# Kernel tuning notes

Hardware: AMD Instinct MI355X
Metric: run time of the kernel (lower is better)

Reference implementation:

```python
import jax, jax.numpy as jnp
import numpy as np

NUM_EMB = 16384
EMB_DIM = 64
BETA = 0.25  # commitment_cost, legacy=True formulation


def _l2norm(x, axis=-1):
    # matches F.normalize(p=2): x / max(||x||, 1e-12)
    n = jnp.sqrt(jnp.sum(x * x, axis=axis, keepdims=True))
    return x / jnp.maximum(n, 1e-12)


def setup_inputs() -> dict:
    key = jax.random.key(0)
    k_z, k_cb, k_w, k_b = jax.random.split(key, 4)
    z = jax.random.normal(k_z, (16, 1024, EMB_DIM), dtype=jnp.float32)
    # frozen codebook: N(0, d^{-0.5})
    codebook = jax.random.normal(k_cb, (NUM_EMB, EMB_DIM), dtype=jnp.float32) * (EMB_DIM ** -0.5)
    # Linear(d, d) default init: U(-1/sqrt(d), 1/sqrt(d))
    lim = 1.0 / np.sqrt(EMB_DIM)
    proj_w = jax.random.uniform(k_w, (EMB_DIM, EMB_DIM), dtype=jnp.float32, minval=-lim, maxval=lim)
    proj_b = jax.random.uniform(k_b, (EMB_DIM,), dtype=jnp.float32, minval=-lim, maxval=lim)
    scale = jnp.float32(10.0)  # l2_norm_scale
    return {"z": z, "codebook": codebook, "proj_w": proj_w, "proj_b": proj_b, "scale": scale}


def reference(z, codebook, proj_w, proj_b, scale):
    B, T, d = z.shape
    zf = z.reshape(-1, d)                                   # [BT, d]
    quant_codebook = codebook @ proj_w.T + proj_b           # [N, d]
    zn = _l2norm(zf)
    cn = _l2norm(quant_codebook)
    distances = -jnp.einsum('bd,nd->bn', zn, cn) * scale    # [BT, N]
    idx = jnp.argmin(distances, axis=1)                     # [BT]
    quantized = quant_codebook[idx].reshape(z.shape)        # [B, T, d]
    sg = jax.lax.stop_gradient
    commitment_loss = jnp.mean((sg(quantized) - z) ** 2)
    codebook_loss = jnp.mean((quantized - sg(z)) ** 2)
    vq_loss = commitment_loss + BETA * codebook_loss        # legacy=True
    quantized_st = z + sg(quantized - z)                    # straight-through
    return quantized_st, vq_loss, idx.reshape(B, T)
```

## Files before the change

### kernel.cpp

```cpp
#include <hip/hip_runtime.h>
#include <hip/hip_bf16.h>


#define NCODES 16384
#define NTOK   16384
#define DIM    64
#define MARGIN_MFMA 8e-3f
#define CAP    16

typedef __attribute__((ext_vector_type(8))) short bf16x8;
typedef __attribute__((ext_vector_type(4))) float f32x4;
#define GLOBAL_AS __attribute__((address_space(1)))
#define LDS_AS    __attribute__((address_space(3)))

__device__ float  g_qcb[NCODES * DIM];
__device__ short  g_cnb[NCODES * DIM];
__device__ short  g_znb[NTOK * DIM];
__device__ unsigned g_topu[NTOK];
__device__ int    g_candcnt[NTOK];
__device__ int    g_cand[NTOK * CAP];
__device__ int    g_wl[NTOK];
__device__ int    g_wln;
__device__ float  g_partial[2048];

__device__ __forceinline__ float wave_sum64(float v) {
#pragma unroll
  for (int o = 32; o > 0; o >>= 1) v += __shfl_xor(v, o, 64);
  return v;
}
__device__ __forceinline__ short f2bf(float f) {
  __hip_bfloat16 h = __float2bfloat16(f);
  return *reinterpret_cast<short*>(&h);
}
__device__ __forceinline__ float bf2f(short s) {
  __hip_bfloat16 h = *reinterpret_cast<__hip_bfloat16*>(&s);
  return __bfloat162float(h);
}
__device__ __forceinline__ void split8(const float* v, bf16x8& hi, bf16x8& lo) {
#pragma unroll
  for (int i = 0; i < 8; ++i) {
    float f = v[i];
    short h = f2bf(f);
    hi[i] = h;
    lo[i] = f2bf(f - bf2f(h));
  }
}
__device__ __forceinline__ void gld_f32(float& dst, const float* addr) {
  asm volatile("global_load_dword %0, %1, off" : "=v"(dst) : "v"(addr));
}
#define WAITV0                                            \
  do {                                                    \
    asm volatile("s_waitcnt vmcnt(0)" ::: "memory");      \
    __builtin_amdgcn_sched_barrier(0);                    \
  } while (0)

__global__ __launch_bounds__(256) void k_prep(const float* __restrict__ cb,
                                              const float* __restrict__ pw,
                                              const float* __restrict__ pb,
                                              const float* __restrict__ z) {
  int tid = threadIdx.x;
  int wave = tid >> 6, lane = tid & 63, quad = lane >> 4, col = lane & 15;
  if (blockIdx.x < 1024) {
    __shared__ float pn[4][16];
    int rowBase = blockIdx.x * 16;
    const float* cr = cb + (size_t)(rowBase + col) * 64 + quad * 8;
    bf16x8 ah0, al0, ah1, al1;
    split8(cr, ah0, al0);
    split8(cr + 32, ah1, al1);
    const f32x4 fz = {0.f, 0.f, 0.f, 0.f};
    int j = wave * 16 + col;
    const float* wr = pw + (size_t)j * 64 + quad * 8;
    bf16x8 bh0, bl0, bh1, bl1;
    split8(wr, bh0, bl0);
    split8(wr + 32, bh1, bl1);
    f32x4 d = __builtin_amdgcn_mfma_f32_16x16x32_bf16(ah0, bh0, fz, 0, 0, 0);
    d = __builtin_amdgcn_mfma_f32_16x16x32_bf16(ah1, bh1, d, 0, 0, 0);
    d = __builtin_amdgcn_mfma_f32_16x16x32_bf16(ah0, bl0, d, 0, 0, 0);
    d = __builtin_amdgcn_mfma_f32_16x16x32_bf16(ah1, bl1, d, 0, 0, 0);
    d = __builtin_amdgcn_mfma_f32_16x16x32_bf16(al0, bh0, d, 0, 0, 0);
    d = __builtin_amdgcn_mfma_f32_16x16x32_bf16(al1, bh1, d, 0, 0, 0);
    float bj = pb[j];
    float vals[4], nr[4];
#pragma unroll
    for (int r = 0; r < 4; ++r) {
      float v = d[r] + bj;
      vals[r] = v;
      nr[r] = v * v;
    }
#pragma unroll
    for (int r = 0; r < 4; ++r) {
      float v = nr[r];
      v += __shfl_xor(v, 1, 64);
      v += __shfl_xor(v, 2, 64);
      v += __shfl_xor(v, 4, 64);
      v += __shfl_xor(v, 8, 64);
      nr[r] = v;
      if (col == 0) pn[wave][quad * 4 + r] = v;
    }
    __syncthreads();
#pragma unroll
    for (int r = 0; r < 4; ++r) {
      int row16 = quad * 4 + r;
      float tot = (pn[0][row16] + pn[1][row16]) + (pn[2][row16] + pn[3][row16]);
      float inv = 1.0f / fmaxf(sqrtf(tot), 1e-12f);
      int row = rowBase + row16;
      g_qcb[(size_t)row * 64 + j] = vals[r];
      g_cnb[(size_t)row * 64 + j] = f2bf(vals[r] * inv);
    }
  } else {
    int zb = blockIdx.x - 1024;
    int zgid = zb * 256 + tid;
    if (zgid < NTOK) { g_topu[zgid] = 0u; g_candcnt[zgid] = 0; }
    if (zgid == 0) g_wln = 0;
    int base = zb * 16;
    int row = base + wave * 4;
#pragma unroll
    for (int r = 0; r < 4; ++r) {
      float v = z[(size_t)(row + r) * 64 + lane];
      float tot = wave_sum64(v * v);
      g_znb[(size_t)(row + r) * 64 + lane] = f2bf(v / fmaxf(sqrtf(tot), 1e-12f));
    }
  }
}

__global__ __launch_bounds__(256) void k_mfma1() {
  __shared__ __align__(16) short smB[2][8192];
  int tid = threadIdx.x;
  int wave = tid >> 6, lane = tid & 63;
  int quad = lane >> 4, col = lane & 15;
  int tokGroup = blockIdx.x >> 4, split = blockIdx.x & 15;
  int tokBase = tokGroup * 256 + wave * 64;

  const short* za = g_znb + (size_t)(tokBase + col) * 64 + quad * 8;
  bf16x8 A0[4], A1[4];
#pragma unroll
  for (int f = 0; f < 4; ++f) {
    A0[f] = *(const bf16x8*)(za + f * 16 * 64);
    A1[f] = *(const bf16x8*)(za + f * 16 * 64 + 32);
  }
  float m[4][4];
#pragma unroll
  for (int f = 0; f < 4; ++f)
#pragma unroll
    for (int r = 0; r < 4; ++r) m[f][r] = -3.0e38f;

  const char* gsplit = (const char*)(g_cnb + (size_t)split * 1024 * 64);
  int x = col & 7;
  int s0off = ((quad ^ x) << 3);
  int s1off = (((4 | quad) ^ x) << 3);
  int goff[4];
#pragma unroll
  for (int i = 0; i < 4; ++i) {
    int cidx = wave * 256 + i * 64 + lane;
    int row = cidx >> 3, sw = cidx & 7;
    goff[i] = row * 128 + ((sw ^ (row & 7)) << 4);
  }

#pragma unroll
  for (int i = 0; i < 4; ++i)
    __builtin_amdgcn_global_load_lds((const GLOBAL_AS void*)(gsplit + goff[i]),
                                     (LDS_AS void*)(&smB[0][wave * 2048 + i * 512]), 16, 0, 0);
  __syncthreads();

  int p = 0;
  for (int s = 0; s < 8; ++s) {
    if (s < 7) {
      const char* gb = gsplit + (size_t)(s + 1) * 16384;
#pragma unroll
      for (int i = 0; i < 4; ++i)
        __builtin_amdgcn_global_load_lds((const GLOBAL_AS void*)(gb + goff[i]),
                                         (LDS_AS void*)(&smB[p ^ 1][wave * 2048 + i * 512]),
                                         16, 0, 0);
    }
    const short* bufp = smB[p];
#pragma unroll
    for (int h = 0; h < 2; ++h) {
      bf16x8 B0[4], B1[4];
#pragma unroll
      for (int t = 0; t < 4; ++t) {
        const short* lb = bufp + ((h * 4 + t) * 16 + col) * 64;
        B0[t] = *(const bf16x8*)(lb + s0off);
        B1[t] = *(const bf16x8*)(lb + s1off);
      }
#pragma unroll
      for (int t = 0; t < 4; ++t) {
#pragma unroll
        for (int f = 0; f < 4; ++f) {
          f32x4 acc = {0.f, 0.f, 0.f, 0.f};
          acc = __builtin_amdgcn_mfma_f32_16x16x32_bf16(A0[f], B0[t], acc, 0, 0, 0);
          acc = __builtin_amdgcn_mfma_f32_16x16x32_bf16(A1[f], B1[t], acc, 0, 0, 0);
#pragma unroll
          for (int r = 0; r < 4; ++r) m[f][r] = fmaxf(m[f][r], acc[r]);
        }
      }
    }
    __syncthreads();
    p ^= 1;
  }

#pragma unroll
  for (int f = 0; f < 4; ++f)
#pragma unroll
    for (int r = 0; r < 4; ++r) {
      float v = m[f][r];
      v = fmaxf(v, __shfl_xor(v, 1, 64));
      v = fmaxf(v, __shfl_xor(v, 2, 64));
      v = fmaxf(v, __shfl_xor(v, 4, 64));
      v = fmaxf(v, __shfl_xor(v, 8, 64));
      if (col == 0) {
        unsigned b = __float_as_uint(v);
        unsigned e = (b & 0x80000000u) ? ~b : (b | 0x80000000u);
        atomicMax(&g_topu[tokBase + f * 16 + quad * 4 + r], e);
      }
    }
}

__global__ __launch_bounds__(256) void k_mfma2() {
  __shared__ __align__(16) short smB[2][8192];
  int tid = threadIdx.x;
  int wave = tid >> 6, lane = tid & 63;
  int quad = lane >> 4, col = lane & 15;
  int tokGroup = blockIdx.x >> 4, split = blockIdx.x & 15;
  int tokBase = tokGroup * 256 + wave * 64;

  const short* za = g_znb + (size_t)(tokBase + col) * 64 + quad * 8;
  bf16x8 A0[4], A1[4];
#pragma unroll
  for (int f = 0; f < 4; ++f) {
    A0[f] = *(const bf16x8*)(za + f * 16 * 64);
    A1[f] = *(const bf16x8*)(za + f * 16 * 64 + 32);
  }
  float th[4][4];
#pragma unroll
  for (int f = 0; f < 4; ++f)
#pragma unroll
    for (int r = 0; r < 4; ++r) {
      unsigned u = g_topu[tokBase + f * 16 + quad * 4 + r];
      unsigned b = (u & 0x80000000u) ? (u & 0x7FFFFFFFu) : ~u;
      th[f][r] = __uint_as_float(b) - MARGIN_MFMA;
    }

  const char* gsplit = (const char*)(g_cnb + (size_t)split * 1024 * 64);
  int x = col & 7;
  int s0off = ((quad ^ x) << 3);
  int s1off = (((4 | quad) ^ x) << 3);
  int goff[4];
#pragma unroll
  for (int i = 0; i < 4; ++i) {
    int cidx = wave * 256 + i * 64 + lane;
    int row = cidx >> 3, sw = cidx & 7;
    goff[i] = row * 128 + ((sw ^ (row & 7)) << 4);
  }

#pragma unroll
  for (int i = 0; i < 4; ++i)
    __builtin_amdgcn_global_load_lds((const GLOBAL_AS void*)(gsplit + goff[i]),
                                     (LDS_AS void*)(&smB[0][wave * 2048 + i * 512]), 16, 0, 0);
  __syncthreads();

  int codeB = split * 1024 + col;
  int p = 0;
  for (int s = 0; s < 8; ++s) {
    if (s < 7) {
      const char* gb = gsplit + (size_t)(s + 1) * 16384;
#pragma unroll
      for (int i = 0; i < 4; ++i)
        __builtin_amdgcn_global_load_lds((const GLOBAL_AS void*)(gb + goff[i]),
                                         (LDS_AS void*)(&smB[p ^ 1][wave * 2048 + i * 512]),
                                         16, 0, 0);
    }
    const short* bufp = smB[p];
#pragma unroll
    for (int h = 0; h < 2; ++h) {
      bf16x8 B0[4], B1[4];
#pragma unroll
      for (int t = 0; t < 4; ++t) {
        const short* lb = bufp + ((h * 4 + t) * 16 + col) * 64;
        B0[t] = *(const bf16x8*)(lb + s0off);
        B1[t] = *(const bf16x8*)(lb + s1off);
      }
#pragma unroll
      for (int t = 0; t < 4; ++t) {
        int code = codeB + s * 128 + (h * 4 + t) * 16;
#pragma unroll
        for (int f = 0; f < 4; ++f) {
          f32x4 acc = {0.f, 0.f, 0.f, 0.f};
          acc = __builtin_amdgcn_mfma_f32_16x16x32_bf16(A0[f], B0[t], acc, 0, 0, 0);
          acc = __builtin_amdgcn_mfma_f32_16x16x32_bf16(A1[f], B1[t], acc, 0, 0, 0);
          float dmax = fmaxf(fmaxf(acc[0] - th[f][0], acc[1] - th[f][1]),
                             fmaxf(acc[2] - th[f][2], acc[3] - th[f][3]));
          if (dmax >= 0.f) {
#pragma unroll
            for (int r = 0; r < 4; ++r) {
              if (acc[r] >= th[f][r]) {
                int tok = tokBase + f * 16 + quad * 4 + r;
                int pos = atomicAdd(&g_candcnt[tok], 1);
                if (pos < CAP) g_cand[tok * CAP + pos] = code;
              }
            }
          }
        }
      }
    }
    __syncthreads();
    p ^= 1;
  }
}

__global__ __launch_bounds__(256) void k_scan() {
  __shared__ int flags[256];
  __shared__ int sbase;
  int tid = threadIdx.x;
  int tok = blockIdx.x * 256 + tid;
  int flag = (g_candcnt[tok] >= 2) ? 1 : 0;
  flags[tid] = flag;
  __syncthreads();
  if (tid == 0) {
    int run = 0;
    for (int i = 0; i < 256; ++i) {
      int f = flags[i];
      flags[i] = run;
      run += f;
    }
    sbase = atomicAdd(&g_wln, run);
  }
  __syncthreads();
  if (flag) g_wl[sbase + flags[tid]] = tok;
}

#define ARB_BODY(CODE)                                                            \
  {                                                                               \
    double s0 = 0.0, s1 = 0.0, s2 = 0.0, s3 = 0.0;                                \
    _Pragma("unroll") for (int kk = 0; kk < 16; ++kk) {                           \
      s0 = fma(WT[kk * 65 + lane], (double)cbl[wave][kk], s0);                    \
      s1 = fma(WT[(kk + 16) * 65 + lane], (double)cbl[wave][kk + 16], s1);        \
      s2 = fma(WT[(kk + 32) * 65 + lane], (double)cbl[wave][kk + 32], s2);        \
      s3 = fma(WT[(kk + 48) * 65 + lane], (double)cbl[wave][kk + 48], s3);        \
    }                                                                             \
    double qc = ((s0 + s1) + (s2 + s3)) + bj;                                     \
    double s = zj * qc, n2 = qc * qc;                                             \
    _Pragma("unroll") for (int o = 32; o > 0; o >>= 1) {                          \
      s += __shfl_xor(s, o, 64);                                                  \
      n2 += __shfl_xor(n2, o, 64);                                                \
    }                                                                             \
    double key = s / fmax(sqrt(n2), 1e-12);                                       \
    if (key > best || (key == best && (CODE) < bi)) { best = key; bi = (CODE); }  \
  }

__global__ __launch_bounds__(256) void k_arb(const float* __restrict__ z,
                                             const float* __restrict__ cb,
                                             const float* __restrict__ pw,
                                             const float* __restrict__ pb) {
  __shared__ double WT[64 * 65];
  __shared__ float cbl[4][64];
  int tid = threadIdx.x;
  int wave = tid >> 6, lane = tid & 63;
  for (int e = tid; e < 4096; e += 256) {
    int j = e >> 6, k = e & 63;
    WT[k * 65 + j] = (double)pw[e];
  }
  __syncthreads();

  int wln = g_wln;
  double bj = (double)pb[lane];
  int gwave = blockIdx.x * 4 + wave;

  for (int e = gwave; e < wln; e += 4096) {
    int tok = g_wl[e];
    int cnt = g_candcnt[tok];
    double zj = (double)z[(size_t)tok * 64 + lane];
    int candv = g_cand[tok * CAP + (lane & 15)];
    double best = -1.0e300;
    int bi = 0x7FFFFFFF;
    int lim = (cnt <= CAP) ? cnt : 0;
    float rA, rB;
    int codeA = 0, codeBv = 0;
    if (lim > 0) {
      codeA = __shfl(candv, 0, 64);
      gld_f32(rA, cb + (size_t)codeA * 64 + lane);
    }
    int c = 0;
    while (c < lim) {
      WAITV0;
      if (c + 1 < lim) {
        codeBv = __shfl(candv, c + 1, 64);
        gld_f32(rB, cb + (size_t)codeBv * 64 + lane);
      }
      cbl[wave][lane] = rA;
      ARB_BODY(codeA);
      ++c;
      if (c >= lim) break;
      WAITV0;
      if (c + 1 < lim) {
        codeA = __shfl(candv, c + 1, 64);
        gld_f32(rA, cb + (size_t)codeA * 64 + lane);
      }
      cbl[wave][lane] = rB;
      ARB_BODY(codeBv);
      ++c;
    }
    if (cnt > CAP) {
      for (int code = 0; code < NCODES; ++code) {
        cbl[wave][lane] = cb[(size_t)code * 64 + lane];
        ARB_BODY(code);
      }
    }
    if (lane == 0) g_cand[tok * CAP] = bi;
  }
}

__global__ __launch_bounds__(256) void k_out(const float* __restrict__ z,
                                             float* __restrict__ out0,
                                             float* __restrict__ out2) {
  __shared__ float ws[4];
  int tid = threadIdx.x;
  int wave = tid >> 6, lane = tid & 63;
  int base = blockIdx.x * 8 + wave * 2;
  int i0 = g_cand[(size_t)base * CAP];
  int i1 = g_cand[(size_t)(base + 1) * CAP];
  float q0 = g_qcb[(size_t)i0 * 64 + lane];
  float z0 = z[(size_t)base * 64 + lane];
  float q1 = g_qcb[(size_t)i1 * 64 + lane];
  float z1 = z[(size_t)(base + 1) * 64 + lane];
  float d0 = q0 - z0;
  float d1 = q1 - z1;
  out0[(size_t)base * 64 + lane] = z0 + d0;
  out0[(size_t)(base + 1) * 64 + lane] = z1 + d1;
  if (lane == 0) {
    out2[base] = (float)i0;
    out2[base + 1] = (float)i1;
  }
  float lsum = fmaf(d0, d0, d1 * d1);
  float tot = wave_sum64(lsum);
  if (lane == 0) ws[wave] = tot;
  __syncthreads();
  if (tid == 0) g_partial[blockIdx.x] = ((ws[0] + ws[1]) + (ws[2] + ws[3]));
}

__global__ void k_loss(float* __restrict__ out1) {
  int lane = threadIdx.x;
  float s = 0.f;
#pragma unroll
  for (int i = 0; i < 32; ++i) s += g_partial[lane + 64 * i];
  s = wave_sum64(s);
  if (lane == 0) out1[0] = 1.25f * s / 1048576.0f;
}

extern "C" void kernel_launch(void* const* d_in, const int* in_sizes, int n_in,
                              void* d_out, int out_size, void* d_ws, size_t ws_size,
                              hipStream_t stream) {
  const float* z = (const float*)d_in[0];
  const float* cb = (const float*)d_in[1];
  const float* pw = (const float*)d_in[2];
  const float* pb = (const float*)d_in[3];

  float* out0 = (float*)d_out;
  float* out1 = out0 + (size_t)NTOK * DIM;
  float* out2 = out1 + 1;

  hipLaunchKernelGGL(k_prep, dim3(2048), dim3(256), 0, stream, cb, pw, pb, z);
  hipLaunchKernelGGL(k_mfma1, dim3(1024), dim3(256), 0, stream);
  hipLaunchKernelGGL(k_mfma2, dim3(1024), dim3(256), 0, stream);
  hipLaunchKernelGGL(k_scan, dim3(64), dim3(256), 0, stream);
  hipLaunchKernelGGL(k_arb, dim3(1024), dim3(256), 0, stream, z, cb, pw, pb);
  hipLaunchKernelGGL(k_out, dim3(2048), dim3(256), 0, stream, z, out0, out2);
  hipLaunchKernelGGL(k_loss, dim3(1), dim3(64), 0, stream, out1);
}
```

Measured before the change: 189.1 us.

## Flatten arbitration into per-candidate work items with atomic max/min winner selection

The exact fp64 re-ranking now treats each (token, candidate) pair as an independent work item for a wave, where before one wave looped over all candidates of a token. A first pass records each token's maximum key with a 64-bit atomicMax on an order-preserving encoding, and handles overflow tokens with a full scan. A second pass recomputes the keys and resolves ties with atomicMin on the code index. This is meant to balance load across waves when candidate counts vary, at the cost of computing every key twice, one extra kernel launch, and added atomics.

```diff
diff --git a/kernel.cpp b/kernel.cpp
--- a/kernel.cpp
+++ b/kernel.cpp
@@ -19,8 +19,12 @@
 __device__ unsigned g_topu[NTOK];
 __device__ int    g_candcnt[NTOK];
 __device__ int    g_cand[NTOK * CAP];
-__device__ int    g_wl[NTOK];
-__device__ int    g_wln;
+__device__ int    g_q[NTOK * CAP];
+__device__ int    g_qn;
+__device__ int    g_ov[NTOK];
+__device__ int    g_ovn;
+__device__ unsigned long long g_keymax[NTOK];
+__device__ int    g_win[NTOK];
 __device__ float  g_partial[2048];
 
 __device__ __forceinline__ float wave_sum64(float v) {
@@ -45,14 +49,28 @@
     lo[i] = f2bf(f - bf2f(h));
   }
 }
-__device__ __forceinline__ void gld_f32(float& dst, const float* addr) {
-  asm volatile("global_load_dword %0, %1, off" : "=v"(dst) : "v"(addr));
-}
-#define WAITV0                                            \
-  do {                                                    \
-    asm volatile("s_waitcnt vmcnt(0)" ::: "memory");      \
-    __builtin_amdgcn_sched_barrier(0);                    \
-  } while (0)
+__device__ __forceinline__ unsigned long long encd(double k) {
+  unsigned long long b = (unsigned long long)__double_as_longlong(k);
+  return (b & 0x8000000000000000ull) ? ~b : (b | 0x8000000000000000ull);
+}
+
+#define ARB_KEY(KEYVAR)                                                           \
+  {                                                                               \
+    double s0 = 0.0, s1 = 0.0, s2 = 0.0, s3 = 0.0;                                \
+    _Pragma("unroll") for (int kk = 0; kk < 16; ++kk) {                           \
+      s0 = fma(WT[kk * 65 + lane], (double)cbl[wave][kk], s0);                    \
+      s1 = fma(WT[(kk + 16) * 65 + lane], (double)cbl[wave][kk + 16], s1);        \
+      s2 = fma(WT[(kk + 32) * 65 + lane], (double)cbl[wave][kk + 32], s2);        \
+      s3 = fma(WT[(kk + 48) * 65 + lane], (double)cbl[wave][kk + 48], s3);        \
+    }                                                                             \
+    double qc = ((s0 + s1) + (s2 + s3)) + bj;                                     \
+    double s = zj * qc, n2 = qc * qc;                                             \
+    _Pragma("unroll") for (int o = 32; o > 0; o >>= 1) {                          \
+      s += __shfl_xor(s, o, 64);                                                  \
+      n2 += __shfl_xor(n2, o, 64);                                                \
+    }                                                                             \
+    KEYVAR = s / fmax(sqrt(n2), 1e-12);                                           \
+  }
 
 __global__ __launch_bounds__(256) void k_prep(const float* __restrict__ cb,
                                               const float* __restrict__ pw,
@@ -111,7 +129,7 @@
     int zb = blockIdx.x - 1024;
     int zgid = zb * 256 + tid;
     if (zgid < NTOK) { g_topu[zgid] = 0u; g_candcnt[zgid] = 0; }
-    if (zgid == 0) g_wln = 0;
+    if (zgid == 0) { g_qn = 0; g_ovn = 0; }
     int base = zb * 16;
     int row = base + wave * 4;
 #pragma unroll
@@ -308,49 +326,43 @@
 }
 
 __global__ __launch_bounds__(256) void k_scan() {
-  __shared__ int flags[256];
-  __shared__ int sbase;
+  __shared__ int pcnt[256];
+  __shared__ int povf[256];
+  __shared__ int qb, ob;
   int tid = threadIdx.x;
   int tok = blockIdx.x * 256 + tid;
-  int flag = (g_candcnt[tok] >= 2) ? 1 : 0;
-  flags[tid] = flag;
+  int cnt = g_candcnt[tok];
+  int np = 0, ov = 0;
+  if (cnt >= 2) {
+    if (cnt <= CAP) np = cnt;
+    else ov = 1;
+    g_keymax[tok] = 0ull;
+    g_win[tok] = 0x7FFFFFFF;
+  }
+  pcnt[tid] = np;
+  povf[tid] = ov;
   __syncthreads();
   if (tid == 0) {
-    int run = 0;
+    int run = 0, rov = 0;
     for (int i = 0; i < 256; ++i) {
-      int f = flags[i];
-      flags[i] = run;
-      run += f;
-    }
-    sbase = atomicAdd(&g_wln, run);
-  }
-  __syncthreads();
-  if (flag) g_wl[sbase + flags[tid]] = tok;
-}
-
-#define ARB_BODY(CODE)                                                            \
-  {                                                                               \
-    double s0 = 0.0, s1 = 0.0, s2 = 0.0, s3 = 0.0;                                \
-    _Pragma("unroll") for (int kk = 0; kk < 16; ++kk) {                           \
-      s0 = fma(WT[kk * 65 + lane], (double)cbl[wave][kk], s0);                    \
-      s1 = fma(WT[(kk + 16) * 65 + lane], (double)cbl[wave][kk + 16], s1);        \
-      s2 = fma(WT[(kk + 32) * 65 + lane], (double)cbl[wave][kk + 32], s2);        \
-      s3 = fma(WT[(kk + 48) * 65 + lane], (double)cbl[wave][kk + 48], s3);        \
-    }                                                                             \
-    double qc = ((s0 + s1) + (s2 + s3)) + bj;                                     \
-    double s = zj * qc, n2 = qc * qc;                                             \
-    _Pragma("unroll") for (int o = 32; o > 0; o >>= 1) {                          \
-      s += __shfl_xor(s, o, 64);                                                  \
-      n2 += __shfl_xor(n2, o, 64);                                                \
-    }                                                                             \
-    double key = s / fmax(sqrt(n2), 1e-12);                                       \
-    if (key > best || (key == best && (CODE) < bi)) { best = key; bi = (CODE); }  \
-  }
-
-__global__ __launch_bounds__(256) void k_arb(const float* __restrict__ z,
-                                             const float* __restrict__ cb,
-                                             const float* __restrict__ pw,
-                                             const float* __restrict__ pb) {
+      int a = pcnt[i]; pcnt[i] = run; run += a;
+      int b = povf[i]; povf[i] = rov; rov += b;
+    }
+    qb = atomicAdd(&g_qn, run);
+    ob = atomicAdd(&g_ovn, rov);
+  }
+  __syncthreads();
+  if (np) {
+    int base = qb + pcnt[tid];
+    for (int i = 0; i < np; ++i) g_q[base + i] = (tok << 4) | i;
+  }
+  if (ov) g_ov[ob + povf[tid]] = tok;
+}
+
+__global__ __launch_bounds__(256) void k_arb1(const float* __restrict__ z,
+                                              const float* __restrict__ cb,
+                                              const float* __restrict__ pw,
+                                              const float* __restrict__ pb) {
   __shared__ double WT[64 * 65];
   __shared__ float cbl[4][64];
   int tid = threadIdx.x;
@@ -361,51 +373,62 @@
   }
   __syncthreads();
 
-  int wln = g_wln;
+  int qn = g_qn, ovn = g_ovn;
   double bj = (double)pb[lane];
   int gwave = blockIdx.x * 4 + wave;
 
-  for (int e = gwave; e < wln; e += 4096) {
-    int tok = g_wl[e];
-    int cnt = g_candcnt[tok];
+  for (int p = gwave; p < qn; p += 4096) {
+    int e = g_q[p];
+    int tok = e >> 4, slot = e & 15;
+    int code = g_cand[tok * CAP + slot];
     double zj = (double)z[(size_t)tok * 64 + lane];
-    int candv = g_cand[tok * CAP + (lane & 15)];
+    cbl[wave][lane] = cb[(size_t)code * 64 + lane];
+    double key;
+    ARB_KEY(key);
+    if (lane == 0) atomicMax(&g_keymax[tok], encd(key));
+  }
+  for (int o = gwave; o < ovn; o += 4096) {
+    int tok = g_ov[o];
+    double zj = (double)z[(size_t)tok * 64 + lane];
     double best = -1.0e300;
     int bi = 0x7FFFFFFF;
-    int lim = (cnt <= CAP) ? cnt : 0;
-    float rA, rB;
-    int codeA = 0, codeBv = 0;
-    if (lim > 0) {
-      codeA = __shfl(candv, 0, 64);
-      gld_f32(rA, cb + (size_t)codeA * 64 + lane);
-    }
-    int c = 0;
-    while (c < lim) {
-      WAITV0;
-      if (c + 1 < lim) {
-        codeBv = __shfl(candv, c + 1, 64);
-        gld_f32(rB, cb + (size_t)codeBv * 64 + lane);
-      }
-      cbl[wave][lane] = rA;
-      ARB_BODY(codeA);
-      ++c;
-      if (c >= lim) break;
-      WAITV0;
-      if (c + 1 < lim) {
-        codeA = __shfl(candv, c + 1, 64);
-        gld_f32(rA, cb + (size_t)codeA * 64 + lane);
-      }
-      cbl[wave][lane] = rB;
-      ARB_BODY(codeBv);
-      ++c;
-    }
-    if (cnt > CAP) {
-      for (int code = 0; code < NCODES; ++code) {
-        cbl[wave][lane] = cb[(size_t)code * 64 + lane];
-        ARB_BODY(code);
-      }
-    }
-    if (lane == 0) g_cand[tok * CAP] = bi;
+    for (int code = 0; code < NCODES; ++code) {
+      cbl[wave][lane] = cb[(size_t)code * 64 + lane];
+      double key;
+      ARB_KEY(key);
+      if (key > best || (key == best && code < bi)) { best = key; bi = code; }
+    }
+    if (lane == 0) g_win[tok] = bi;
+  }
+}
+
+__global__ __launch_bounds__(256) void k_arb2(const float* __restrict__ z,
+                                              const float* __restrict__ cb,
+                                              const float* __restrict__ pw,
+                                              const float* __restrict__ pb) {
+  __shared__ double WT[64 * 65];
+  __shared__ float cbl[4][64];
+  int tid = threadIdx.x;
+  int wave = tid >> 6, lane = tid & 63;
+  for (int e = tid; e < 4096; e += 256) {
+    int j = e >> 6, k = e & 63;
+    WT[k * 65 + j] = (double)pw[e];
+  }
+  __syncthreads();
+
+  int qn = g_qn;
+  double bj = (double)pb[lane];
+  int gwave = blockIdx.x * 4 + wave;
+
+  for (int p = gwave; p < qn; p += 4096) {
+    int e = g_q[p];
+    int tok = e >> 4, slot = e & 15;
+    int code = g_cand[tok * CAP + slot];
+    double zj = (double)z[(size_t)tok * 64 + lane];
+    cbl[wave][lane] = cb[(size_t)code * 64 + lane];
+    double key;
+    ARB_KEY(key);
+    if (lane == 0 && encd(key) == g_keymax[tok]) atomicMin(&g_win[tok], code);
   }
 }
 
@@ -416,8 +439,10 @@
   int tid = threadIdx.x;
   int wave = tid >> 6, lane = tid & 63;
   int base = blockIdx.x * 8 + wave * 2;
-  int i0 = g_cand[(size_t)base * CAP];
-  int i1 = g_cand[(size_t)(base + 1) * CAP];
+  int c0 = g_candcnt[base];
+  int c1 = g_candcnt[base + 1];
+  int i0 = (c0 >= 2) ? g_win[base] : g_cand[(size_t)base * CAP];
+  int i1 = (c1 >= 2) ? g_win[base + 1] : g_cand[(size_t)(base + 1) * CAP];
   float q0 = g_qcb[(size_t)i0 * 64 + lane];
   float z0 = z[(size_t)base * 64 + lane];
   float q1 = g_qcb[(size_t)i1 * 64 + lane];
@@ -462,7 +487,8 @@
   hipLaunchKernelGGL(k_mfma1, dim3(1024), dim3(256), 0, stream);
   hipLaunchKernelGGL(k_mfma2, dim3(1024), dim3(256), 0, stream);
   hipLaunchKernelGGL(k_scan, dim3(64), dim3(256), 0, stream);
-  hipLaunchKernelGGL(k_arb, dim3(1024), dim3(256), 0, stream, z, cb, pw, pb);
+  hipLaunchKernelGGL(k_arb1, dim3(1024), dim3(256), 0, stream, z, cb, pw, pb);
+  hipLaunchKernelGGL(k_arb2, dim3(1024), dim3(256), 0, stream, z, cb, pw, pb);
   hipLaunchKernelGGL(k_out, dim3(2048), dim3(256), 0, stream, z, out0, out2);
   hipLaunchKernelGGL(k_loss, dim3(1), dim3(64), 0, stream, out1);
 }
```

After: 222.2 us. 1.18x slower.
